# Kernel optimization log

Measured on AMD Instinct MI355X. Metric: run time of the kernel, lower is better.

## Reference

```python
import jax, jax.numpy as jnp
import numpy as np

N = 100000      # nodes
E = 1600000     # edges
D_IN = 128
D_HID = 128
D_OUT = 128
K = 6           # Taylor truncation order for exp-series diffusion
GAMMA = 0.0     # self-loop weight from init_kwargs


def setup_inputs() -> dict:
    key = jax.random.key(0)
    ks = jax.random.split(key, 6)
    h = jax.random.normal(ks[0], (N, D_IN), dtype=jnp.float32)
    edge_index = jax.random.randint(ks[1], (2, E), 0, N, dtype=jnp.int32)
    s_in = 1.0 / np.sqrt(D_IN)
    s_hid = 1.0 / np.sqrt(D_HID)
    W_in = (jax.random.normal(ks[2], (D_IN, D_HID), dtype=jnp.float32) * s_in)
    b_in = jnp.zeros((D_HID,), jnp.float32)
    W1 = (jax.random.normal(ks[3], (D_HID, D_HID), dtype=jnp.float32) * s_hid)
    b1 = jnp.zeros((D_HID,), jnp.float32)
    W2 = (jax.random.normal(ks[4], (D_HID, D_OUT), dtype=jnp.float32) * s_hid)
    b2 = jnp.zeros((D_OUT,), jnp.float32)
    return {"h": h, "edge_index": edge_index, "W_in": W_in, "b_in": b_in,
            "W1": W1, "b1": b1, "W2": W2, "b2": b2}


def _linear_diffusion(h, src, dst, gamma):
    """Truncated Taylor series of exp(A_hat + gamma*I) @ h, where A_hat is the
    in-degree (row) normalized adjacency given by the edge list (src -> dst)."""
    ones = jnp.ones((E,), h.dtype)
    deg = jax.ops.segment_sum(ones, dst, num_segments=N)          # in-degree [N]
    w = (1.0 / jnp.maximum(deg, 1.0))[dst]                         # per-edge norm [E]
    out = h
    term = h
    for i in range(1, K + 1):
        # one hop of normalized adjacency: gather src feats, scale, scatter to dst
        agg = jax.ops.segment_sum(term[src] * w[:, None], dst, num_segments=N)
        term = (agg + gamma * term) / i
        out = out + term
    return out


def reference(h, edge_index, W_in, b_in, W1, b1, W2, b2):
    src, dst = edge_index[0], edge_index[1]
    x = jax.nn.silu(h @ W_in + b_in)              # fc_in + activation
    x = _linear_diffusion(x, src, dst, GAMMA)     # graph diffusion
    x = jax.nn.silu(x @ W1 + b1)                  # fc_out: Linear + SiLU
    return x @ W2 + b2                            # fc_out: final Linear
```

## Files before the change

### kernel.cpp

```cpp
#include <hip/hip_runtime.h>

#define D 128
#define K_ORDER 6
#define NB_SHIFT 9
#define CPT 8

typedef __attribute__((ext_vector_type(8))) short short8;
typedef __attribute__((ext_vector_type(4))) float f32x4;
typedef __attribute__((ext_vector_type(4))) unsigned uint4v;

__device__ __forceinline__ float silu_f(float x) {
    return x / (1.0f + __expf(-x));
}

__device__ __forceinline__ unsigned pack_bf2(float lo, float hi) {
    unsigned ul = __float_as_uint(lo);
    unsigned uh = __float_as_uint(hi);
    ul = (ul + 0x7fffu + ((ul >> 16) & 1u)) >> 16;
    uh = (uh + 0x7fffu + ((uh >> 16) & 1u)) & 0xffff0000u;
    return uh | ul;
}

__device__ __forceinline__ unsigned short bf16_of(float f) {
    unsigned u = __float_as_uint(f);
    u = (u + 0x7fffu + ((u >> 16) & 1u)) >> 16;
    return (unsigned short)u;
}


__global__ __launch_bounds__(256) void bucket_hist_kernel(
        const int* __restrict__ dst, int* __restrict__ bucket_cnt, int e, int nb) {
    __shared__ int hist[256];
    for (int i = threadIdx.x; i < 256; i += 256) hist[i] = 0;
    __syncthreads();
    int i0 = blockIdx.x * (256 * CPT) + threadIdx.x;
    #pragma unroll
    for (int k = 0; k < CPT; ++k) {
        int idx = i0 + k * 256;
        if (idx < e) atomicAdd(&hist[dst[idx] >> NB_SHIFT], 1);
    }
    __syncthreads();
    for (int i = threadIdx.x; i < nb; i += 256) {
        int h = hist[i];
        if (h) atomicAdd(&bucket_cnt[i], h);
    }
}

__global__ __launch_bounds__(256) void scan_buckets_kernel(
        const int* __restrict__ bucket_cnt, int* __restrict__ bucket_base,
        int* __restrict__ bin_cur, int nb) {
    __shared__ int lds[256];
    int v = (threadIdx.x < (unsigned)nb) ? bucket_cnt[threadIdx.x] : 0;
    lds[threadIdx.x] = v;
    __syncthreads();
    #pragma unroll
    for (int off = 1; off < 256; off <<= 1) {
        int t = (threadIdx.x >= (unsigned)off) ? lds[threadIdx.x - off] : 0;
        __syncthreads();
        lds[threadIdx.x] += t;
        __syncthreads();
    }
    if (threadIdx.x < (unsigned)nb) {
        int b = lds[threadIdx.x] - v;
        bucket_base[threadIdx.x] = b;
        bin_cur[threadIdx.x] = b;
    }
}

__global__ __launch_bounds__(256) void bin_edges_kernel(
        const int* __restrict__ src, const int* __restrict__ dst,
        int* __restrict__ bin_cur, unsigned* __restrict__ binned, int e, int nb) {
    __shared__ int hist[256];
    __shared__ int base[256];
    for (int i = threadIdx.x; i < 256; i += 256) hist[i] = 0;
    __syncthreads();

    int e0 = blockIdx.x * (256 * CPT) + threadIdx.x;
    int myb[CPT], myoff[CPT];
    unsigned mypk[CPT];
    #pragma unroll
    for (int k = 0; k < CPT; ++k) {
        int idx = e0 + k * 256;
        bool ok = idx < e;
        int d = ok ? dst[idx] : 0;
        int s = ok ? src[idx] : 0;
        int b = d >> NB_SHIFT;
        int off = ok ? atomicAdd(&hist[b], 1) : 0;
        myb[k] = b; myoff[k] = off;
        mypk[k] = ((unsigned)s << NB_SHIFT) | (unsigned)(d & ((1 << NB_SHIFT) - 1));
    }
    __syncthreads();
    for (int i = threadIdx.x; i < nb; i += 256) {
        int h = hist[i];
        base[i] = h ? atomicAdd(&bin_cur[i], h) : 0;
    }
    __syncthreads();
    #pragma unroll
    for (int k = 0; k < CPT; ++k) {
        int idx = e0 + k * 256;
        if (idx < e)
            binned[(size_t)base[myb[k]] + myoff[k]] = mypk[k];
    }
}

__global__ __launch_bounds__(512) void bucket_csr_kernel(
        const unsigned* __restrict__ binned, const int* __restrict__ bucket_base,
        int* __restrict__ row_ptr, int* __restrict__ ssrc, int n, int e, int nb) {
    __shared__ int hist[512];
    __shared__ int pfx[512];
    const int b = blockIdx.x;
    const int node0 = b << NB_SHIFT;
    const int beg = bucket_base[b];
    const int end = (b + 1 < nb) ? bucket_base[b + 1] : e;

    hist[threadIdx.x] = 0;
    __syncthreads();
    for (int j = beg + (int)threadIdx.x; j < end; j += 512)
        atomicAdd(&hist[binned[j] & 511u], 1);
    __syncthreads();

    int v = hist[threadIdx.x];
    pfx[threadIdx.x] = v;
    __syncthreads();
    #pragma unroll
    for (int off = 1; off < 512; off <<= 1) {
        int t = (threadIdx.x >= (unsigned)off) ? pfx[threadIdx.x - off] : 0;
        __syncthreads();
        pfx[threadIdx.x] += t;
        __syncthreads();
    }
    int excl = pfx[threadIdx.x] - v;

    int node = node0 + (int)threadIdx.x;
    if (node < n) row_ptr[node] = beg + excl;
    if (b == nb - 1 && threadIdx.x == 0) row_ptr[n] = e;
    __syncthreads();

    hist[threadIdx.x] = 0;
    pfx[threadIdx.x] = excl;
    __syncthreads();

    for (int j = beg + (int)threadIdx.x; j < end; j += 512) {
        unsigned p = binned[j];
        int dl = (int)(p & 511u);
        int pos = beg + pfx[dl] + atomicAdd(&hist[dl], 1);
        ssrc[pos] = (int)(p >> NB_SHIFT);
    }
}

template <int ALAY, bool SILU, int OLAY>
__global__ __launch_bounds__(256) void gemm_mfma_kernel(
        const void* __restrict__ Ap, const float* __restrict__ W,
        const float* __restrict__ bias, void* __restrict__ outp, int nrows) {
    constexpr int LDW = 136;
    __shared__ unsigned short sWt[128 * LDW];

    for (int i = threadIdx.x; i < 128 * 128; i += 256) {
        int c = i & 127, k = i >> 7;
        sWt[c * LDW + k] = bf16_of(W[(size_t)k * 128 + c]);
    }
    __syncthreads();

    const int wave = threadIdx.x >> 6;
    const int lane = threadIdx.x & 63;
    const int lhi = lane >> 4;
    const int llo = lane & 15;

    const int rbase = blockIdx.x * 128 + wave * 32;

    f32x4 acc[2][8] = {};

    #pragma unroll
    for (int ks = 0; ks < 4; ++ks) {
        const int k0 = ks * 32 + lhi * 8;
        short8 afrag[2];
        #pragma unroll
        for (int rt = 0; rt < 2; ++rt) {
            int r = rbase + rt * 16 + llo;
            if (r < nrows) {
                if (ALAY == 0) {
                    const float* ap = (const float*)Ap + (size_t)r * 128 + k0;
                    float4 f0 = *(const float4*)ap;
                    float4 f1 = *(const float4*)(ap + 4);
                    union { unsigned u[4]; short8 s; } cvt;
                    cvt.u[0] = pack_bf2(f0.x, f0.y);
                    cvt.u[1] = pack_bf2(f0.z, f0.w);
                    cvt.u[2] = pack_bf2(f1.x, f1.y);
                    cvt.u[3] = pack_bf2(f1.z, f1.w);
                    afrag[rt] = cvt.s;
                } else {
                    afrag[rt] = *(const short8*)((const unsigned short*)Ap + (size_t)r * 128 + k0);
                }
            } else {
                afrag[rt] = short8{0, 0, 0, 0, 0, 0, 0, 0};
            }
        }
        #pragma unroll
        for (int ct = 0; ct < 8; ++ct) {
            short8 bfrag = *(const short8*)(sWt + (ct * 16 + llo) * LDW + k0);
            acc[0][ct] = __builtin_amdgcn_mfma_f32_16x16x32_bf16(afrag[0], bfrag, acc[0][ct], 0, 0, 0);
            acc[1][ct] = __builtin_amdgcn_mfma_f32_16x16x32_bf16(afrag[1], bfrag, acc[1][ct], 0, 0, 0);
        }
    }

    float bv[8];
    #pragma unroll
    for (int ct = 0; ct < 8; ++ct) bv[ct] = bias[ct * 16 + llo];

    #pragma unroll
    for (int rt = 0; rt < 2; ++rt) {
        int rb = rbase + rt * 16 + lhi * 4;
        #pragma unroll
        for (int reg = 0; reg < 4; ++reg) {
            int r = rb + reg;
            if (r >= nrows) continue;
            if (OLAY == 1) {
                float* orow = (float*)outp + (size_t)r * 128;
                #pragma unroll
                for (int ct = 0; ct < 8; ++ct) {
                    float v = acc[rt][ct][reg] + bv[ct];
                    if (SILU) v = silu_f(v);
                    orow[ct * 16 + llo] = v;
                }
            } else {
                unsigned short* orow = (unsigned short*)outp + (size_t)r * 128;
                #pragma unroll
                for (int ct = 0; ct < 8; ++ct) {
                    float v = acc[rt][ct][reg] + bv[ct];
                    if (SILU) v = silu_f(v);
                    orow[ct * 16 + llo] = bf16_of(v);
                }
            }
        }
    }
}


#define ACC8(v)                                          \
    do {                                                 \
        a0 += __uint_as_float((v).x << 16);              \
        a1 += __uint_as_float((v).x & 0xffff0000u);      \
        a2 += __uint_as_float((v).y << 16);              \
        a3 += __uint_as_float((v).y & 0xffff0000u);      \
        a4 += __uint_as_float((v).z << 16);              \
        a5 += __uint_as_float((v).z & 0xffff0000u);      \
        a6 += __uint_as_float((v).w << 16);              \
        a7 += __uint_as_float((v).w & 0xffff0000u);      \
    } while (0)

__global__ __launch_bounds__(256) void horner_bf_kernel(
        const uint4v* __restrict__ u, const uint4v* __restrict__ xb,
        uint4v* __restrict__ u_next,
        const int* __restrict__ row_ptr, const int* __restrict__ ssrc,
        float inv_i, int nrows) {
    const int lt = threadIdx.x & 15;
    const int row = blockIdx.x * 16 + (threadIdx.x >> 4);
    if (row >= nrows) return;

    const int beg = row_ptr[row];
    const int end = row_ptr[row + 1];
    const int deg = end - beg;

    float a0 = 0.f, a1 = 0.f, a2 = 0.f, a3 = 0.f,
          a4 = 0.f, a5 = 0.f, a6 = 0.f, a7 = 0.f;

    int j = beg;
    for (; j + 7 < end; j += 8) {
        int s0 = ssrc[j + 0], s1 = ssrc[j + 1], s2 = ssrc[j + 2], s3 = ssrc[j + 3];
        int s4 = ssrc[j + 4], s5 = ssrc[j + 5], s6 = ssrc[j + 6], s7 = ssrc[j + 7];
        uint4v t0 = u[(size_t)s0 * 16 + lt];
        uint4v t1 = u[(size_t)s1 * 16 + lt];
        uint4v t2 = u[(size_t)s2 * 16 + lt];
        uint4v t3 = u[(size_t)s3 * 16 + lt];
        uint4v t4 = u[(size_t)s4 * 16 + lt];
        uint4v t5 = u[(size_t)s5 * 16 + lt];
        uint4v t6 = u[(size_t)s6 * 16 + lt];
        uint4v t7 = u[(size_t)s7 * 16 + lt];
        ACC8(t0); ACC8(t1); ACC8(t2); ACC8(t3);
        ACC8(t4); ACC8(t5); ACC8(t6); ACC8(t7);
    }
    for (; j + 3 < end; j += 4) {
        int s0 = ssrc[j + 0], s1 = ssrc[j + 1], s2 = ssrc[j + 2], s3 = ssrc[j + 3];
        uint4v t0 = u[(size_t)s0 * 16 + lt];
        uint4v t1 = u[(size_t)s1 * 16 + lt];
        uint4v t2 = u[(size_t)s2 * 16 + lt];
        uint4v t3 = u[(size_t)s3 * 16 + lt];
        ACC8(t0); ACC8(t1); ACC8(t2); ACC8(t3);
    }
    for (; j < end; ++j) {
        uint4v t0 = u[(size_t)ssrc[j] * 16 + lt];
        ACC8(t0);
    }

    const float scale = inv_i / (float)(deg > 1 ? deg : 1);
    const size_t o = (size_t)row * 16 + lt;
    uint4v xv = __builtin_nontemporal_load(xb + o);
    float r0 = fmaf(a0, scale, __uint_as_float(xv.x << 16));
    float r1 = fmaf(a1, scale, __uint_as_float(xv.x & 0xffff0000u));
    float r2 = fmaf(a2, scale, __uint_as_float(xv.y << 16));
    float r3 = fmaf(a3, scale, __uint_as_float(xv.y & 0xffff0000u));
    float r4 = fmaf(a4, scale, __uint_as_float(xv.z << 16));
    float r5 = fmaf(a5, scale, __uint_as_float(xv.z & 0xffff0000u));
    float r6 = fmaf(a6, scale, __uint_as_float(xv.w << 16));
    float r7 = fmaf(a7, scale, __uint_as_float(xv.w & 0xffff0000u));
    uint4v ov;
    ov.x = pack_bf2(r0, r1);
    ov.y = pack_bf2(r2, r3);
    ov.z = pack_bf2(r4, r5);
    ov.w = pack_bf2(r6, r7);
    __builtin_nontemporal_store(ov, u_next + o);
}


extern "C" void kernel_launch(void* const* d_in, const int* in_sizes, int n_in,
                              void* d_out, int out_size, void* d_ws, size_t ws_size,
                              hipStream_t stream) {
    const float* h      = (const float*)d_in[0];
    const int*   eidx   = (const int*)d_in[1];
    const float* W_in   = (const float*)d_in[2];
    const float* b_in   = (const float*)d_in[3];
    const float* W1     = (const float*)d_in[4];
    const float* b1     = (const float*)d_in[5];
    const float* W2     = (const float*)d_in[6];
    const float* b2     = (const float*)d_in[7];
    float* out = (float*)d_out;

    const int N = in_sizes[0] / D;
    const int E = in_sizes[1] / 2;
    const int NB = (N + (1 << NB_SHIFT) - 1) >> NB_SHIFT;

    const int* e_src = eidx;
    const int* e_dst = eidx + E;

    unsigned short* Xb = (unsigned short*)d_ws;
    unsigned short* U0 = Xb + (size_t)N * 128;
    unsigned short* U1 = U0 + (size_t)N * 128;
    unsigned* binned   = (unsigned*)(U1 + (size_t)N * 128);
    int* ssrc        = (int*)(binned + E);
    int* row_ptr     = ssrc + E;
    int* bucket_cnt  = row_ptr + N + 1;
    int* bucket_base = bucket_cnt + 256;
    int* bin_cur     = bucket_base + 256;

    hipMemsetAsync(bucket_cnt, 0, 256 * sizeof(int), stream);

    const int eb = (E + 256 * CPT - 1) / (256 * CPT);
    bucket_hist_kernel<<<eb, 256, 0, stream>>>(e_dst, bucket_cnt, E, NB);
    scan_buckets_kernel<<<1, 256, 0, stream>>>(bucket_cnt, bucket_base, bin_cur, NB);
    bin_edges_kernel<<<eb, 256, 0, stream>>>(e_src, e_dst, bin_cur, binned, E, NB);
    bucket_csr_kernel<<<NB, 512, 0, stream>>>(binned, bucket_base, row_ptr, ssrc, N, E, NB);

    const int gb = (N + 127) / 128;
    gemm_mfma_kernel<0, true, 0><<<gb, 256, 0, stream>>>(h, W_in, b_in, Xb, N);

    const int db = (N + 15) / 16;
    const uint4v* Xv = (const uint4v*)Xb;
    uint4v* U0v = (uint4v*)U0;
    uint4v* U1v = (uint4v*)U1;
    horner_bf_kernel<<<db, 256, 0, stream>>>(Xv, Xv, U0v, row_ptr, ssrc, 1.0f / 6.0f, N);
    horner_bf_kernel<<<db, 256, 0, stream>>>(U0v, Xv, U1v, row_ptr, ssrc, 1.0f / 5.0f, N);
    horner_bf_kernel<<<db, 256, 0, stream>>>(U1v, Xv, U0v, row_ptr, ssrc, 1.0f / 4.0f, N);
    horner_bf_kernel<<<db, 256, 0, stream>>>(U0v, Xv, U1v, row_ptr, ssrc, 1.0f / 3.0f, N);
    horner_bf_kernel<<<db, 256, 0, stream>>>(U1v, Xv, U0v, row_ptr, ssrc, 1.0f / 2.0f, N);
    horner_bf_kernel<<<db, 256, 0, stream>>>(U0v, Xv, U1v, row_ptr, ssrc, 1.0f, N);

    gemm_mfma_kernel<1, true, 0><<<gb, 256, 0, stream>>>(U1, W1, b1, U0, N);
    gemm_mfma_kernel<1, false, 1><<<gb, 256, 0, stream>>>(U0, W2, b2, out, N);
}
```

Measured before the change: 532.3 us.

## Sort rows by degree for diffusion load balance and pretranspose weights once

```diff
diff --git a/kernel.cpp b/kernel.cpp
--- a/kernel.cpp
+++ b/kernel.cpp
@@ -148,19 +148,66 @@
     }
 }
 
+
+__global__ __launch_bounds__(512) void deg_hist_kernel(
+        const int* __restrict__ row_ptr, int* __restrict__ dhist, int n) {
+    __shared__ int h[512];
+    h[threadIdx.x] = 0;
+    __syncthreads();
+    int i = blockIdx.x * 512 + threadIdx.x;
+    if (i < n) {
+        int d = row_ptr[i + 1] - row_ptr[i];
+        if (d > 511) d = 511;
+        atomicAdd(&h[d], 1);
+    }
+    __syncthreads();
+    int v = h[threadIdx.x];
+    if (v) atomicAdd(&dhist[threadIdx.x], v);
+}
+
+__global__ __launch_bounds__(512) void deg_scan_kernel(
+        const int* __restrict__ dhist, int* __restrict__ dcur) {
+    __shared__ int lds[512];
+    int v = dhist[threadIdx.x];
+    lds[threadIdx.x] = v;
+    __syncthreads();
+    #pragma unroll
+    for (int off = 1; off < 512; off <<= 1) {
+        int t = (threadIdx.x >= (unsigned)off) ? lds[threadIdx.x - off] : 0;
+        __syncthreads();
+        lds[threadIdx.x] += t;
+        __syncthreads();
+    }
+    dcur[threadIdx.x] = lds[threadIdx.x] - v;
+}
+
+__global__ __launch_bounds__(512) void deg_scatter_kernel(
+        const int* __restrict__ row_ptr, int* __restrict__ dcur,
+        int* __restrict__ perm, int n) {
+    int i = blockIdx.x * 512 + threadIdx.x;
+    if (i < n) {
+        int d = row_ptr[i + 1] - row_ptr[i];
+        if (d > 511) d = 511;
+        int pos = atomicAdd(&dcur[d], 1);
+        perm[pos] = i;
+    }
+}
+
+__global__ __launch_bounds__(256) void transpose_w_kernel(
+        const float* __restrict__ W0, const float* __restrict__ W1,
+        const float* __restrict__ W2, unsigned short* __restrict__ Wt) {
+    int i = blockIdx.x * 256 + threadIdx.x;
+    int w = i >> 14;
+    int r = i & 16383;
+    int k = r >> 7, c = r & 127;
+    const float* W = (w == 0) ? W0 : ((w == 1) ? W1 : W2);
+    Wt[(size_t)w * 16384 + c * 128 + k] = bf16_of(W[r]);
+}
+
 template <int ALAY, bool SILU, int OLAY>
 __global__ __launch_bounds__(256) void gemm_mfma_kernel(
-        const void* __restrict__ Ap, const float* __restrict__ W,
+        const void* __restrict__ Ap, const unsigned short* __restrict__ Wt,
         const float* __restrict__ bias, void* __restrict__ outp, int nrows) {
-    constexpr int LDW = 136;
-    __shared__ unsigned short sWt[128 * LDW];
-
-    for (int i = threadIdx.x; i < 128 * 128; i += 256) {
-        int c = i & 127, k = i >> 7;
-        sWt[c * LDW + k] = bf16_of(W[(size_t)k * 128 + c]);
-    }
-    __syncthreads();
-
     const int wave = threadIdx.x >> 6;
     const int lane = threadIdx.x & 63;
     const int lhi = lane >> 4;
@@ -197,7 +244,7 @@
         }
         #pragma unroll
         for (int ct = 0; ct < 8; ++ct) {
-            short8 bfrag = *(const short8*)(sWt + (ct * 16 + llo) * LDW + k0);
+            short8 bfrag = *(const short8*)(Wt + (size_t)(ct * 16 + llo) * 128 + k0);
             acc[0][ct] = __builtin_amdgcn_mfma_f32_16x16x32_bf16(afrag[0], bfrag, acc[0][ct], 0, 0, 0);
             acc[1][ct] = __builtin_amdgcn_mfma_f32_16x16x32_bf16(afrag[1], bfrag, acc[1][ct], 0, 0, 0);
         }
@@ -252,10 +299,12 @@
         const uint4v* __restrict__ u, const uint4v* __restrict__ xb,
         uint4v* __restrict__ u_next,
         const int* __restrict__ row_ptr, const int* __restrict__ ssrc,
+        const int* __restrict__ perm,
         float inv_i, int nrows) {
     const int lt = threadIdx.x & 15;
-    const int row = blockIdx.x * 16 + (threadIdx.x >> 4);
-    if (row >= nrows) return;
+    const int gid = blockIdx.x * 16 + (threadIdx.x >> 4);
+    if (gid >= nrows) return;
+    const int row = perm[gid];
 
     const int beg = row_ptr[row];
     const int end = row_ptr[row + 1];
@@ -294,7 +343,7 @@
 
     const float scale = inv_i / (float)(deg > 1 ? deg : 1);
     const size_t o = (size_t)row * 16 + lt;
-    uint4v xv = __builtin_nontemporal_load(xb + o);
+    uint4v xv = xb[o];
     float r0 = fmaf(a0, scale, __uint_as_float(xv.x << 16));
     float r1 = fmaf(a1, scale, __uint_as_float(xv.x & 0xffff0000u));
     float r2 = fmaf(a2, scale, __uint_as_float(xv.y << 16));
@@ -335,14 +384,18 @@
     unsigned short* Xb = (unsigned short*)d_ws;
     unsigned short* U0 = Xb + (size_t)N * 128;
     unsigned short* U1 = U0 + (size_t)N * 128;
-    unsigned* binned   = (unsigned*)(U1 + (size_t)N * 128);
+    unsigned short* Wt = U1 + (size_t)N * 128;
+    unsigned* binned   = (unsigned*)(Wt + 3 * 16384);
     int* ssrc        = (int*)(binned + E);
     int* row_ptr     = ssrc + E;
     int* bucket_cnt  = row_ptr + N + 1;
-    int* bucket_base = bucket_cnt + 256;
+    int* dhist       = bucket_cnt + 256;
+    int* dcur        = dhist + 512;
+    int* bucket_base = dcur + 512;
     int* bin_cur     = bucket_base + 256;
-
-    hipMemsetAsync(bucket_cnt, 0, 256 * sizeof(int), stream);
+    int* perm        = bin_cur + 256;
+
+    hipMemsetAsync(bucket_cnt, 0, (256 + 512) * sizeof(int), stream);
 
     const int eb = (E + 256 * CPT - 1) / (256 * CPT);
     bucket_hist_kernel<<<eb, 256, 0, stream>>>(e_dst, bucket_cnt, E, NB);
@@ -350,20 +403,27 @@
     bin_edges_kernel<<<eb, 256, 0, stream>>>(e_src, e_dst, bin_cur, binned, E, NB);
     bucket_csr_kernel<<<NB, 512, 0, stream>>>(binned, bucket_base, row_ptr, ssrc, N, E, NB);
 
+    const int nrb = (N + 511) / 512;
+    deg_hist_kernel<<<nrb, 512, 0, stream>>>(row_ptr, dhist, N);
+    deg_scan_kernel<<<1, 512, 0, stream>>>(dhist, dcur);
+    deg_scatter_kernel<<<nrb, 512, 0, stream>>>(row_ptr, dcur, perm, N);
+
+    transpose_w_kernel<<<192, 256, 0, stream>>>(W_in, W1, W2, Wt);
+
     const int gb = (N + 127) / 128;
-    gemm_mfma_kernel<0, true, 0><<<gb, 256, 0, stream>>>(h, W_in, b_in, Xb, N);
+    gemm_mfma_kernel<0, true, 0><<<gb, 256, 0, stream>>>(h, Wt, b_in, Xb, N);
 
     const int db = (N + 15) / 16;
     const uint4v* Xv = (const uint4v*)Xb;
     uint4v* U0v = (uint4v*)U0;
     uint4v* U1v = (uint4v*)U1;
-    horner_bf_kernel<<<db, 256, 0, stream>>>(Xv, Xv, U0v, row_ptr, ssrc, 1.0f / 6.0f, N);
-    horner_bf_kernel<<<db, 256, 0, stream>>>(U0v, Xv, U1v, row_ptr, ssrc, 1.0f / 5.0f, N);
-    horner_bf_kernel<<<db, 256, 0, stream>>>(U1v, Xv, U0v, row_ptr, ssrc, 1.0f / 4.0f, N);
-    horner_bf_kernel<<<db, 256, 0, stream>>>(U0v, Xv, U1v, row_ptr, ssrc, 1.0f / 3.0f, N);
-    horner_bf_kernel<<<db, 256, 0, stream>>>(U1v, Xv, U0v, row_ptr, ssrc, 1.0f / 2.0f, N);
-    horner_bf_kernel<<<db, 256, 0, stream>>>(U0v, Xv, U1v, row_ptr, ssrc, 1.0f, N);
-
-    gemm_mfma_kernel<1, true, 0><<<gb, 256, 0, stream>>>(U1, W1, b1, U0, N);
-    gemm_mfma_kernel<1, false, 1><<<gb, 256, 0, stream>>>(U0, W2, b2, out, N);
-}
+    horner_bf_kernel<<<db, 256, 0, stream>>>(Xv, Xv, U0v, row_ptr, ssrc, perm, 1.0f / 6.0f, N);
+    horner_bf_kernel<<<db, 256, 0, stream>>>(U0v, Xv, U1v, row_ptr, ssrc, perm, 1.0f / 5.0f, N);
+    horner_bf_kernel<<<db, 256, 0, stream>>>(U1v, Xv, U0v, row_ptr, ssrc, perm, 1.0f / 4.0f, N);
+    horner_bf_kernel<<<db, 256, 0, stream>>>(U0v, Xv, U1v, row_ptr, ssrc, perm, 1.0f / 3.0f, N);
+    horner_bf_kernel<<<db, 256, 0, stream>>>(U1v, Xv, U0v, row_ptr, ssrc, perm, 1.0f / 2.0f, N);
+    horner_bf_kernel<<<db, 256, 0, stream>>>(U0v, Xv, U1v, row_ptr, ssrc, perm, 1.0f, N);
+
+    gemm_mfma_kernel<1, true, 0><<<gb, 256, 0, stream>>>(U1, Wt + 16384, b1, U0, N);
+    gemm_mfma_kernel<1, false, 1><<<gb, 256, 0, stream>>>(U0, Wt + 2 * 16384, b2, out, N);
+}
```

After: 834.6 us. 56.8% more time.

## Pad CSR rows to multiples of eight and pre-transpose weights once

Applied to the files above, without the earlier changes.

```diff
diff --git a/kernel.cpp b/kernel.cpp
--- a/kernel.cpp
+++ b/kernel.cpp
@@ -4,6 +4,7 @@
 #define K_ORDER 6
 #define NB_SHIFT 9
 #define CPT 8
+#define BPAD 4096
 
 typedef __attribute__((ext_vector_type(8))) short short8;
 typedef __attribute__((ext_vector_type(4))) float f32x4;
@@ -105,13 +106,15 @@
 
 __global__ __launch_bounds__(512) void bucket_csr_kernel(
         const unsigned* __restrict__ binned, const int* __restrict__ bucket_base,
-        int* __restrict__ row_ptr, int* __restrict__ ssrc, int n, int e, int nb) {
+        int* __restrict__ row_start, int* __restrict__ degv,
+        int* __restrict__ ssrc, int n, int e, int nb) {
     __shared__ int hist[512];
     __shared__ int pfx[512];
     const int b = blockIdx.x;
     const int node0 = b << NB_SHIFT;
     const int beg = bucket_base[b];
     const int end = (b + 1 < nb) ? bucket_base[b + 1] : e;
+    const int pbeg = ((beg + 7) & ~7) + b * BPAD;
 
     hist[threadIdx.x] = 0;
     __syncthreads();
@@ -119,8 +122,9 @@
         atomicAdd(&hist[binned[j] & 511u], 1);
     __syncthreads();
 
-    int v = hist[threadIdx.x];
-    pfx[threadIdx.x] = v;
+    const int mydeg = hist[threadIdx.x];
+    const int mypc = (mydeg + 7) & ~7;
+    pfx[threadIdx.x] = mypc;
     __syncthreads();
     #pragma unroll
     for (int off = 1; off < 512; off <<= 1) {
@@ -129,38 +133,48 @@
         pfx[threadIdx.x] += t;
         __syncthreads();
     }
-    int excl = pfx[threadIdx.x] - v;
-
-    int node = node0 + (int)threadIdx.x;
-    if (node < n) row_ptr[node] = beg + excl;
-    if (b == nb - 1 && threadIdx.x == 0) row_ptr[n] = e;
-    __syncthreads();
-
+    const int myexcl = pfx[threadIdx.x] - mypc;
+
+    const int node = node0 + (int)threadIdx.x;
+    if (node < n) {
+        row_start[node] = pbeg + myexcl;
+        degv[node] = mydeg;
+    }
+    __syncthreads();
+
+    pfx[threadIdx.x] = myexcl;
     hist[threadIdx.x] = 0;
-    pfx[threadIdx.x] = excl;
     __syncthreads();
 
     for (int j = beg + (int)threadIdx.x; j < end; j += 512) {
         unsigned p = binned[j];
         int dl = (int)(p & 511u);
-        int pos = beg + pfx[dl] + atomicAdd(&hist[dl], 1);
+        int pos = pbeg + pfx[dl] + atomicAdd(&hist[dl], 1);
         ssrc[pos] = (int)(p >> NB_SHIFT);
     }
+    __syncthreads();
+
+    if (node < n) {
+        int base = pbeg + myexcl;
+        for (int k = mydeg; k < mypc; ++k) ssrc[base + k] = n;
+    }
+}
+
+__global__ __launch_bounds__(256) void transpose_w_kernel(
+        const float* __restrict__ W0, const float* __restrict__ W1,
+        const float* __restrict__ W2, unsigned short* __restrict__ Wt) {
+    int i = blockIdx.x * 256 + threadIdx.x;
+    int w = i >> 14;
+    int r = i & 16383;
+    int k = r >> 7, c = r & 127;
+    const float* W = (w == 0) ? W0 : ((w == 1) ? W1 : W2);
+    Wt[(size_t)w * 16384 + c * 128 + k] = bf16_of(W[r]);
 }
 
 template <int ALAY, bool SILU, int OLAY>
 __global__ __launch_bounds__(256) void gemm_mfma_kernel(
-        const void* __restrict__ Ap, const float* __restrict__ W,
+        const void* __restrict__ Ap, const unsigned short* __restrict__ Wt,
         const float* __restrict__ bias, void* __restrict__ outp, int nrows) {
-    constexpr int LDW = 136;
-    __shared__ unsigned short sWt[128 * LDW];
-
-    for (int i = threadIdx.x; i < 128 * 128; i += 256) {
-        int c = i & 127, k = i >> 7;
-        sWt[c * LDW + k] = bf16_of(W[(size_t)k * 128 + c]);
-    }
-    __syncthreads();
-
     const int wave = threadIdx.x >> 6;
     const int lane = threadIdx.x & 63;
     const int lhi = lane >> 4;
@@ -197,7 +211,7 @@
         }
         #pragma unroll
         for (int ct = 0; ct < 8; ++ct) {
-            short8 bfrag = *(const short8*)(sWt + (ct * 16 + llo) * LDW + k0);
+            short8 bfrag = *(const short8*)(Wt + (size_t)(ct * 16 + llo) * 128 + k0);
             acc[0][ct] = __builtin_amdgcn_mfma_f32_16x16x32_bf16(afrag[0], bfrag, acc[0][ct], 0, 0, 0);
             acc[1][ct] = __builtin_amdgcn_mfma_f32_16x16x32_bf16(afrag[1], bfrag, acc[1][ct], 0, 0, 0);
         }
@@ -251,50 +265,38 @@
 __global__ __launch_bounds__(256) void horner_bf_kernel(
         const uint4v* __restrict__ u, const uint4v* __restrict__ xb,
         uint4v* __restrict__ u_next,
-        const int* __restrict__ row_ptr, const int* __restrict__ ssrc,
+        const int* __restrict__ row_start, const int* __restrict__ degv,
+        const int* __restrict__ ssrc,
         float inv_i, int nrows) {
     const int lt = threadIdx.x & 15;
     const int row = blockIdx.x * 16 + (threadIdx.x >> 4);
     if (row >= nrows) return;
 
-    const int beg = row_ptr[row];
-    const int end = row_ptr[row + 1];
-    const int deg = end - beg;
+    const int beg = row_start[row];
+    const int deg = degv[row];
+    const int pend = beg + ((deg + 7) & ~7);
 
     float a0 = 0.f, a1 = 0.f, a2 = 0.f, a3 = 0.f,
           a4 = 0.f, a5 = 0.f, a6 = 0.f, a7 = 0.f;
 
-    int j = beg;
-    for (; j + 7 < end; j += 8) {
-        int s0 = ssrc[j + 0], s1 = ssrc[j + 1], s2 = ssrc[j + 2], s3 = ssrc[j + 3];
-        int s4 = ssrc[j + 4], s5 = ssrc[j + 5], s6 = ssrc[j + 6], s7 = ssrc[j + 7];
-        uint4v t0 = u[(size_t)s0 * 16 + lt];
-        uint4v t1 = u[(size_t)s1 * 16 + lt];
-        uint4v t2 = u[(size_t)s2 * 16 + lt];
-        uint4v t3 = u[(size_t)s3 * 16 + lt];
-        uint4v t4 = u[(size_t)s4 * 16 + lt];
-        uint4v t5 = u[(size_t)s5 * 16 + lt];
-        uint4v t6 = u[(size_t)s6 * 16 + lt];
-        uint4v t7 = u[(size_t)s7 * 16 + lt];
+    for (int j = beg; j < pend; j += 8) {
+        int4 sA = *(const int4*)(ssrc + j);
+        int4 sB = *(const int4*)(ssrc + j + 4);
+        uint4v t0 = u[(size_t)sA.x * 16 + lt];
+        uint4v t1 = u[(size_t)sA.y * 16 + lt];
+        uint4v t2 = u[(size_t)sA.z * 16 + lt];
+        uint4v t3 = u[(size_t)sA.w * 16 + lt];
+        uint4v t4 = u[(size_t)sB.x * 16 + lt];
+        uint4v t5 = u[(size_t)sB.y * 16 + lt];
+        uint4v t6 = u[(size_t)sB.z * 16 + lt];
+        uint4v t7 = u[(size_t)sB.w * 16 + lt];
         ACC8(t0); ACC8(t1); ACC8(t2); ACC8(t3);
         ACC8(t4); ACC8(t5); ACC8(t6); ACC8(t7);
     }
-    for (; j + 3 < end; j += 4) {
-        int s0 = ssrc[j + 0], s1 = ssrc[j + 1], s2 = ssrc[j + 2], s3 = ssrc[j + 3];
-        uint4v t0 = u[(size_t)s0 * 16 + lt];
-        uint4v t1 = u[(size_t)s1 * 16 + lt];
-        uint4v t2 = u[(size_t)s2 * 16 + lt];
-        uint4v t3 = u[(size_t)s3 * 16 + lt];
-        ACC8(t0); ACC8(t1); ACC8(t2); ACC8(t3);
-    }
-    for (; j < end; ++j) {
-        uint4v t0 = u[(size_t)ssrc[j] * 16 + lt];
-        ACC8(t0);
-    }
 
     const float scale = inv_i / (float)(deg > 1 ? deg : 1);
     const size_t o = (size_t)row * 16 + lt;
-    uint4v xv = __builtin_nontemporal_load(xb + o);
+    uint4v xv = xb[o];
     float r0 = fmaf(a0, scale, __uint_as_float(xv.x << 16));
     float r1 = fmaf(a1, scale, __uint_as_float(xv.x & 0xffff0000u));
     float r2 = fmaf(a2, scale, __uint_as_float(xv.y << 16));
@@ -308,7 +310,7 @@
     ov.y = pack_bf2(r2, r3);
     ov.z = pack_bf2(r4, r5);
     ov.w = pack_bf2(r6, r7);
-    __builtin_nontemporal_store(ov, u_next + o);
+    u_next[o] = ov;
 }
 
 
@@ -332,38 +334,48 @@
     const int* e_src = eidx;
     const int* e_dst = eidx + E;
 
+    const size_t rowsz = (size_t)(N + 1) * 128;
+
     unsigned short* Xb = (unsigned short*)d_ws;
-    unsigned short* U0 = Xb + (size_t)N * 128;
-    unsigned short* U1 = U0 + (size_t)N * 128;
-    unsigned* binned   = (unsigned*)(U1 + (size_t)N * 128);
+    unsigned short* U0 = Xb + rowsz;
+    unsigned short* U1 = U0 + rowsz;
+    unsigned short* Wt = U1 + rowsz;
+    unsigned* binned   = (unsigned*)(Wt + 3 * 16384);
     int* ssrc        = (int*)(binned + E);
-    int* row_ptr     = ssrc + E;
-    int* bucket_cnt  = row_ptr + N + 1;
+    int* row_start   = ssrc + E + NB * BPAD + 16;
+    int* degv        = row_start + N;
+    int* bucket_cnt  = degv + N;
     int* bucket_base = bucket_cnt + 256;
     int* bin_cur     = bucket_base + 256;
 
     hipMemsetAsync(bucket_cnt, 0, 256 * sizeof(int), stream);
+    hipMemsetAsync(Xb + (size_t)N * 128, 0, 256, stream);
+    hipMemsetAsync(U0 + (size_t)N * 128, 0, 256, stream);
+    hipMemsetAsync(U1 + (size_t)N * 128, 0, 256, stream);
 
     const int eb = (E + 256 * CPT - 1) / (256 * CPT);
     bucket_hist_kernel<<<eb, 256, 0, stream>>>(e_dst, bucket_cnt, E, NB);
     scan_buckets_kernel<<<1, 256, 0, stream>>>(bucket_cnt, bucket_base, bin_cur, NB);
     bin_edges_kernel<<<eb, 256, 0, stream>>>(e_src, e_dst, bin_cur, binned, E, NB);
-    bucket_csr_kernel<<<NB, 512, 0, stream>>>(binned, bucket_base, row_ptr, ssrc, N, E, NB);
+    bucket_csr_kernel<<<NB, 512, 0, stream>>>(binned, bucket_base, row_start, degv,
+                                              ssrc, N, E, NB);
+
+    transpose_w_kernel<<<192, 256, 0, stream>>>(W_in, W1, W2, Wt);
 
     const int gb = (N + 127) / 128;
-    gemm_mfma_kernel<0, true, 0><<<gb, 256, 0, stream>>>(h, W_in, b_in, Xb, N);
+    gemm_mfma_kernel<0, true, 0><<<gb, 256, 0, stream>>>(h, Wt, b_in, Xb, N);
 
     const int db = (N + 15) / 16;
     const uint4v* Xv = (const uint4v*)Xb;
     uint4v* U0v = (uint4v*)U0;
     uint4v* U1v = (uint4v*)U1;
-    horner_bf_kernel<<<db, 256, 0, stream>>>(Xv, Xv, U0v, row_ptr, ssrc, 1.0f / 6.0f, N);
-    horner_bf_kernel<<<db, 256, 0, stream>>>(U0v, Xv, U1v, row_ptr, ssrc, 1.0f / 5.0f, N);
-    horner_bf_kernel<<<db, 256, 0, stream>>>(U1v, Xv, U0v, row_ptr, ssrc, 1.0f / 4.0f, N);
-    horner_bf_kernel<<<db, 256, 0, stream>>>(U0v, Xv, U1v, row_ptr, ssrc, 1.0f / 3.0f, N);
-    horner_bf_kernel<<<db, 256, 0, stream>>>(U1v, Xv, U0v, row_ptr, ssrc, 1.0f / 2.0f, N);
-    horner_bf_kernel<<<db, 256, 0, stream>>>(U0v, Xv, U1v, row_ptr, ssrc, 1.0f, N);
-
-    gemm_mfma_kernel<1, true, 0><<<gb, 256, 0, stream>>>(U1, W1, b1, U0, N);
-    gemm_mfma_kernel<1, false, 1><<<gb, 256, 0, stream>>>(U0, W2, b2, out, N);
-}
+    horner_bf_kernel<<<db, 256, 0, stream>>>(Xv, Xv, U0v, row_start, degv, ssrc, 1.0f / 6.0f, N);
+    horner_bf_kernel<<<db, 256, 0, stream>>>(U0v, Xv, U1v, row_start, degv, ssrc, 1.0f / 5.0f, N);
+    horner_bf_kernel<<<db, 256, 0, stream>>>(U1v, Xv, U0v, row_start, degv, ssrc, 1.0f / 4.0f, N);
+    horner_bf_kernel<<<db, 256, 0, stream>>>(U0v, Xv, U1v, row_start, degv, ssrc, 1.0f / 3.0f, N);
+    horner_bf_kernel<<<db, 256, 0, stream>>>(U1v, Xv, U0v, row_start, degv, ssrc, 1.0f / 2.0f, N);
+    horner_bf_kernel<<<db, 256, 0, stream>>>(U0v, Xv, U1v, row_start, degv, ssrc, 1.0f, N);
+
+    gemm_mfma_kernel<1, true, 0><<<gb, 256, 0, stream>>>(U1, Wt + 16384, b1, U0, N);
+    gemm_mfma_kernel<1, false, 1><<<gb, 256, 0, stream>>>(U0, Wt + 2 * 16384, b2, out, N);
+}
```

Result: no change. 532.2 us (-0.0%).
